# Kernel optimization log

Hardware: AMD Instinct MI355X
Metric: run time of the kernel (lower is better)

The kernel has to match this reference:

```python
import math
import jax, jax.numpy as jnp
import numpy as np

B, M, N, D, H = 64, 5, 1000, 128, 8
KS = D // H
TANH_CLIP = 10.0

def setup_inputs() -> dict:
    key = jax.random.key(0)
    ks = jax.random.split(key, 12)
    mask = jax.random.randint(ks[8], (B, M, N), 0, 2).astype(bool)
    mask = mask.at[:, 0, 0].set(True)  # guarantee at least one feasible action per batch row
    return {
        'node_embeddings': jax.random.normal(ks[0], (B, N, D), jnp.float32),
        'fixed_context': jax.random.normal(ks[1], (B, 1, D), jnp.float32),
        'prev_node_embeddings': jax.random.normal(ks[2], (B, M, D), jnp.float32),
        'node_dynamic_features': jax.random.normal(ks[3], (B, M, N, 8), jnp.float32),
        'vehicle_dynamic_features': jax.random.normal(ks[4], (B, M, 3), jnp.float32),
        'glimpse_V_static': jax.random.normal(ks[5], (H, B, 1, N, KS), jnp.float32),
        'glimpse_K_static': jax.random.normal(ks[6], (H, B, 1, N, KS), jnp.float32),
        'logit_K_static': jax.random.normal(ks[7], (B, 1, N, D), jnp.float32),
        'feasibility_mask': mask,
        'W_pcv': jax.random.normal(ks[9], (D, D + 3), jnp.float32) * 0.05,
        'W_pns': jax.random.normal(ks[10], (3 * D, 8), jnp.float32) * 0.05,
        'po_weight': jax.random.normal(ks[11], (D, D), jnp.float32) * 0.05,
    }

def reference(node_embeddings, fixed_context, prev_node_embeddings,
              node_dynamic_features, vehicle_dynamic_features,
              glimpse_V_static, glimpse_K_static, logit_K_static,
              feasibility_mask, W_pcv, W_pns, po_weight):
    # current vehicle state projection: [B,M,D]
    cvs = jnp.concatenate([prev_node_embeddings, vehicle_dynamic_features], axis=-1)
    proj_cvs = cvs @ W_pcv.T
    # dynamic node embeddings: [B,M,N,3D] -> three [B,M,N,D] chunks
    nde = node_dynamic_features @ W_pns.T
    gVd, gKd, lKd = jnp.split(nde, 3, axis=-1)
    # make heads: [B,M,N,D] -> [H,B,M,N,KS]
    def mh(x):
        return x.reshape(B, M, N, H, KS).transpose(3, 0, 1, 2, 4)
    glimpse_V = glimpse_V_static + mh(gVd)  # [H,B,M,N,KS]
    glimpse_K = glimpse_K_static + mh(gKd)
    logit_K = logit_K_static + lKd          # [B,M,N,D]
    query = fixed_context + proj_cvs        # [B,M,D]
    Q = query.reshape(B, M, H, KS).transpose(2, 0, 1, 3)  # [H,B,M,KS]
    mask_log = jnp.log(feasibility_mask.astype(jnp.float32))  # [B,M,N]
    compat = jnp.einsum('hbmk,hbmnk->hbmn', Q, glimpse_K) / math.sqrt(KS)
    compat = compat + mask_log[None]
    # softmax over joint vehicle*node axis
    attn = jax.nn.softmax(compat.reshape(H, B, M * N), axis=-1).reshape(H, B, M, N)
    heads = jnp.einsum('hbmn,hbmnk->hbmk', attn, glimpse_V)  # [H,B,M,KS]
    concat = heads.transpose(1, 2, 0, 3).reshape(B, M, D)
    final_Q = concat @ po_weight.T          # [B,M,D]
    logits = jnp.einsum('bmd,bmnd->bmn', final_Q, logit_K) / math.sqrt(D)
    logits = jnp.tanh(logits) * TANH_CLIP + mask_log
    probs = jax.nn.softmax(logits.reshape(B, M * N), axis=-1)
    return probs
```

## Files before the change

kernel.cpp:

```cpp
#include <hip/hip_runtime.h>
#include <cstddef>

#define BB 64
#define MM 5
#define NN 1000
#define DD 128
#define HH 8
#define KSZ 16
#define NCH 4
#define CH2 250
#define NC3 8
#define CH3 125
#define INV_SQRT_D 0.08838834764831845f

__device__ __forceinline__ float tanh_fast(float x) {
  float e = __expf(2.f * x);
  return 1.f - 2.f / (e + 1.f);
}

__global__ __launch_bounds__(256) void k1_query(
    const float* __restrict__ fc, const float* __restrict__ pne,
    const float* __restrict__ vdf, const float* __restrict__ wpcv,
    const float* __restrict__ wpns, const int* __restrict__ mask,
    float* __restrict__ q_ws, float* __restrict__ qw_ws,
    unsigned int* __restrict__ pmask)
{
  const int t = threadIdx.x;
  if (blockIdx.x >= BB * MM) {
    const int b = blockIdx.x - BB * MM;
    const int* mb = mask + (size_t)(b * MM) * NN;
    for (int n = t; n < NN; n += 256) {
      unsigned int pm = 0;
#pragma unroll
      for (int m = 0; m < MM; ++m) pm |= (mb[m * NN + n] != 0 ? 1u : 0u) << m;
      pmask[b * NN + n] = pm;
    }
    return;
  }
  const int bm = blockIdx.x;
  const int b = bm / MM;
  const int k = t & 15, gid = t >> 4;
  __shared__ float qsh[DD];

  float cvr[9];
  const float* pner = pne + (size_t)bm * DD;
#pragma unroll
  for (int jp = 0; jp < 8; ++jp) cvr[jp] = pner[k + 16 * jp];
  cvr[8] = (k < 3) ? vdf[bm * 3 + k] : 0.f;

#pragma unroll 2
  for (int dd = 0; dd < 8; ++dd) {
    const int d = gid + 16 * dd;
    const float* wrow = wpcv + d * 131;
    float p = 0.f;
#pragma unroll
    for (int jp = 0; jp < 8; ++jp) p = fmaf(cvr[jp], wrow[k + 16 * jp], p);
    if (k < 3) p = fmaf(cvr[8], wrow[128 + k], p);
    p += __shfl_xor(p, 1); p += __shfl_xor(p, 2);
    p += __shfl_xor(p, 4); p += __shfl_xor(p, 8);
    if (k == 0) {
      const float q = 0.25f * (p + fc[b * DD + d]);
      qsh[d] = q;
      q_ws[(size_t)bm * DD + d] = q;
    }
  }
  __syncthreads();
  if (t < 64) {
    const int h = t >> 3, f = t & 7;
    float acc = 0.f;
#pragma unroll
    for (int kk = 0; kk < KSZ; ++kk)
      acc = fmaf(qsh[h * KSZ + kk], wpns[(DD + h * KSZ + kk) * 8 + f], acc);
    qw_ws[(b * HH + h) * 40 + (bm % MM) * 8 + f] = acc;
  }
}

__global__ __launch_bounds__(256, 3) void k2_attn(
    const float* __restrict__ ndf, const float* __restrict__ gV,
    const float* __restrict__ gK, const unsigned int* __restrict__ pmask,
    const float* __restrict__ q_ws, const float* __restrict__ qw_ws,
    float* __restrict__ part)
{
  const int blk = blockIdx.x;
  const int c = blk & 3;
  const int h = (blk >> 2) & 7;
  const int b = blk >> 5;
  const int t = threadIdx.x;
  const int k = t & 3, gid = t >> 2;
  const int n0 = c * CH2;

  const float* kbase = gK + ((size_t)(h * BB + b) * NN + n0) * KSZ;
  const float* vbase = gV + ((size_t)(h * BB + b) * NN + n0) * KSZ;
  const float* nbase = ndf + ((size_t)(b * MM) * NN + n0) * 8;
  const unsigned int* pmb = pmask + b * NN + n0;

  float4 kv[4], vv[4];
  float2 ndv[4][MM];
  unsigned int pm[4];
#pragma unroll
  for (int i = 0; i < 4; ++i) {
    const int nl = gid + 64 * i;
    const bool valid = (nl < CH2);
    const int nc = valid ? nl : 0;
    pm[i] = valid ? pmb[nc] : 0u;
    kv[i] = *(const float4*)(kbase + nc * KSZ + 4 * k);
    vv[i] = *(const float4*)(vbase + nc * KSZ + 4 * k);
#pragma unroll
    for (int m = 0; m < MM; ++m)
      ndv[i][m] = *(const float2*)(nbase + ((size_t)m * NN + nc) * 8 + 2 * k);
  }

  float4 qr[MM];
  float2 qwr[MM];
#pragma unroll
  for (int m = 0; m < MM; ++m) {
    qr[m] = *(const float4*)(q_ws + (size_t)(b * MM + m) * DD + h * KSZ + 4 * k);
    qwr[m] = *(const float2*)(qw_ws + (b * HH + h) * 40 + m * 8 + 2 * k);
  }
  float4 hacc[MM] = {};
  float2 afv[MM] = {};
  float lsum = 0.f;

#pragma unroll
  for (int i = 0; i < 4; ++i) {
#pragma unroll
    for (int m = 0; m < MM; ++m) {
      float p = kv[i].x * qr[m].x + kv[i].y * qr[m].y
              + kv[i].z * qr[m].z + kv[i].w * qr[m].w
              + ndv[i][m].x * qwr[m].x + ndv[i][m].y * qwr[m].y;
      p += __shfl_xor(p, 1); p += __shfl_xor(p, 2);
      const float e = ((pm[i] >> m) & 1u) ? __expf(p) : 0.f;
      hacc[m].x = fmaf(e, vv[i].x, hacc[m].x);
      hacc[m].y = fmaf(e, vv[i].y, hacc[m].y);
      hacc[m].z = fmaf(e, vv[i].z, hacc[m].z);
      hacc[m].w = fmaf(e, vv[i].w, hacc[m].w);
      afv[m].x = fmaf(e, ndv[i][m].x, afv[m].x);
      afv[m].y = fmaf(e, ndv[i][m].y, afv[m].y);
      lsum += e;
    }
  }

#pragma unroll
  for (int m = 0; m < MM; ++m) {
#pragma unroll
    for (int off = 4; off <= 32; off <<= 1) {
      hacc[m].x += __shfl_xor(hacc[m].x, off);
      hacc[m].y += __shfl_xor(hacc[m].y, off);
      hacc[m].z += __shfl_xor(hacc[m].z, off);
      hacc[m].w += __shfl_xor(hacc[m].w, off);
      afv[m].x += __shfl_xor(afv[m].x, off);
      afv[m].y += __shfl_xor(afv[m].y, off);
    }
  }
#pragma unroll
  for (int off = 4; off <= 32; off <<= 1) lsum += __shfl_xor(lsum, off);

  __shared__ float redh[4][MM][KSZ];
  __shared__ float redaf[4][MM][8];
  __shared__ float reds[4];
  const int w = t >> 6;
  if ((t & 63) < 4) {
    const int kk = t & 3;
#pragma unroll
    for (int m = 0; m < MM; ++m) {
      redh[w][m][4 * kk + 0] = hacc[m].x;
      redh[w][m][4 * kk + 1] = hacc[m].y;
      redh[w][m][4 * kk + 2] = hacc[m].z;
      redh[w][m][4 * kk + 3] = hacc[m].w;
      redaf[w][m][2 * kk + 0] = afv[m].x;
      redaf[w][m][2 * kk + 1] = afv[m].y;
    }
  }
  if ((t & 63) == 0) reds[w] = lsum;
  __syncthreads();
  float* P = part + (size_t)blk * 128;
  if (t < 80) {
    const int m = t >> 4, kk = t & 15;
    P[t] = redh[0][m][kk] + redh[1][m][kk] + redh[2][m][kk] + redh[3][m][kk];
  } else if (t < 120) {
    const int r = t - 80, m = r >> 3, f = r & 7;
    P[80 + r] = redaf[0][m][f] + redaf[1][m][f] + redaf[2][m][f] + redaf[3][m][f];
  } else if (t == 120) {
    P[120] = reds[0] + reds[1] + reds[2] + reds[3];
  }
}

__global__ __launch_bounds__(512) void k3_logits(
    const float* __restrict__ ndf, const float* __restrict__ lK,
    const unsigned int* __restrict__ pmask, const float* __restrict__ part,
    const float* __restrict__ wpns, const float* __restrict__ po,
    float* __restrict__ out, float* __restrict__ stats)
{
  const int b = blockIdx.x >> 3;
  const int c = blockIdx.x & 7;
  const int t = threadIdx.x;

  __shared__ float pos[DD][129];
  __shared__ float rgs[HH];
  __shared__ float afs[HH][MM][8];
  __shared__ float cs[MM][DD];
  __shared__ float fqs[MM][DD];
  __shared__ float fw[MM][8];
  __shared__ float wred[8];

  for (int i = t; i < DD * DD / 4; i += 512) {
    const float4 v = ((const float4*)po)[i];
    const int r = (i * 4) >> 7, cc = (i * 4) & 127;
    pos[r][cc] = v.x; pos[r][cc + 1] = v.y; pos[r][cc + 2] = v.z; pos[r][cc + 3] = v.w;
  }
  const float* pb = part + (size_t)b * 32 * 128;
  if (t < HH) {
    float s = 0.f;
#pragma unroll
    for (int cc = 0; cc < NCH; ++cc) s += pb[(t * 4 + cc) * 128 + 120];
    rgs[t] = 1.f / s;
  }
  if (t < HH * MM * 8) {
    const int h = t / 40, r = t % 40;
    float a = 0.f;
#pragma unroll
    for (int cc = 0; cc < NCH; ++cc) a += pb[(h * 4 + cc) * 128 + 80 + r];
    afs[h][r >> 3][r & 7] = a;
  }
  __syncthreads();
  for (int idx = t; idx < MM * DD; idx += 512) {
    const int m = idx >> 7, d = idx & 127, h = d >> 4;
    float a = 0.f;
#pragma unroll
    for (int cc = 0; cc < NCH; ++cc) a += pb[(h * 4 + cc) * 128 + m * 16 + (d & 15)];
    float cf = 0.f;
#pragma unroll
    for (int f = 0; f < 8; ++f) cf = fmaf(wpns[d * 8 + f], afs[h][m][f], cf);
    cs[m][d] = (a + cf) * rgs[h];
  }
  __syncthreads();
  for (int idx = t; idx < MM * DD; idx += 512) {
    const int m = idx >> 7, d = idx & 127;
    float acc = 0.f;
#pragma unroll 8
    for (int j = 0; j < DD; ++j) acc = fmaf(cs[m][j], pos[d][j], acc);
    fqs[m][d] = acc * INV_SQRT_D;
  }
  __syncthreads();
  if (t < MM * 8) {
    const int m = t >> 3, f = t & 7;
    float acc = 0.f;
#pragma unroll 16
    for (int d = 0; d < DD; ++d) acc = fmaf(fqs[m][d], wpns[(2 * DD + d) * 8 + f], acc);
    fw[m][f] = acc;
  }
  __syncthreads();

  const int k = t & 15, gid = t >> 4;
  const int n0 = c * CH3;
  float4 fqr[MM][2];
  float fwr[MM];
#pragma unroll
  for (int m = 0; m < MM; ++m) {
    fqr[m][0] = *(const float4*)(&fqs[m][8 * k]);
    fqr[m][1] = *(const float4*)(&fqs[m][8 * k + 4]);
    fwr[m] = fw[m][k & 7];
  }
  float lsum = 0.f;

#pragma unroll
  for (int i = 0; i < 4; ++i) {
    const int nl = gid + 32 * i;
    const bool valid = (nl < CH3);
    const int n = n0 + (valid ? nl : 0);
    const unsigned int pm = valid ? pmask[b * NN + n] : 0u;
    const float* lkr = lK + ((size_t)b * NN + n) * DD;
    const float4 l0 = *(const float4*)(lkr + 8 * k);
    const float4 l1 = *(const float4*)(lkr + 8 * k + 4);
    float ndv[MM];
#pragma unroll
    for (int m = 0; m < MM; ++m)
      ndv[m] = (k < 8) ? ndf[((size_t)(b * MM + m) * NN + n) * 8 + k] : 0.f;
#pragma unroll
    for (int m = 0; m < MM; ++m) {
      float p = l0.x * fqr[m][0].x + l0.y * fqr[m][0].y
              + l0.z * fqr[m][0].z + l0.w * fqr[m][0].w
              + l1.x * fqr[m][1].x + l1.y * fqr[m][1].y
              + l1.z * fqr[m][1].z + l1.w * fqr[m][1].w
              + ndv[m] * fwr[m];
      p += __shfl_xor(p, 1); p += __shfl_xor(p, 2);
      p += __shfl_xor(p, 4); p += __shfl_xor(p, 8);
      const float e = ((pm >> m) & 1u) ? __expf(tanh_fast(p) * 10.f) : 0.f;
      if (valid) {
        lsum += e;
        if (k == 0) out[(size_t)(b * MM + m) * NN + n] = e;
      }
    }
  }
  lsum += __shfl_xor(lsum, 16);
  lsum += __shfl_xor(lsum, 32);
  if ((t & 63) == 0) wred[t >> 6] = lsum;
  __syncthreads();
  if (t == 0) {
    float s = 0.f;
#pragma unroll
    for (int w = 0; w < 8; ++w) s += wred[w];
    stats[b * NC3 + c] = s;
  }
}

__global__ __launch_bounds__(256) void k4_probs(
    const float* __restrict__ stats, float* __restrict__ out)
{
  const int bm = blockIdx.x;
  const int b = bm / MM;
  const int t = threadIdx.x;
  float s = 0.f;
#pragma unroll
  for (int c = 0; c < NC3; ++c) s += stats[b * NC3 + c];
  const float scale = 1.f / s;
  if (t < 250) {
    float4* p = (float4*)(out + (size_t)bm * NN);
    float4 v = p[t];
    v.x *= scale; v.y *= scale; v.z *= scale; v.w *= scale;
    p[t] = v;
  }
}

extern "C" void kernel_launch(void* const* d_in, const int* in_sizes, int n_in,
                              void* d_out, int out_size, void* d_ws, size_t ws_size,
                              hipStream_t stream) {
  const float* fc   = (const float*)d_in[1];
  const float* pne  = (const float*)d_in[2];
  const float* ndf  = (const float*)d_in[3];
  const float* vdf  = (const float*)d_in[4];
  const float* gV   = (const float*)d_in[5];
  const float* gK   = (const float*)d_in[6];
  const float* lK   = (const float*)d_in[7];
  const int*   mask = (const int*)d_in[8];
  const float* wpcv = (const float*)d_in[9];
  const float* wpns = (const float*)d_in[10];
  const float* po   = (const float*)d_in[11];

  float* q_ws  = (float*)d_ws;
  float* qw_ws = q_ws + BB * MM * DD;
  float* part  = qw_ws + BB * HH * MM * 8;
  float* stats = part + (size_t)BB * HH * NCH * 128;
  unsigned int* pmask = (unsigned int*)(stats + BB * NC3);
  float* out   = (float*)d_out;

  k1_query<<<BB * MM + BB, 256, 0, stream>>>(fc, pne, vdf, wpcv, wpns, mask,
                                             q_ws, qw_ws, pmask);
  k2_attn<<<BB * HH * NCH, 256, 0, stream>>>(ndf, gV, gK, pmask, q_ws, qw_ws, part);
  k3_logits<<<BB * NC3, 512, 0, stream>>>(ndf, lK, pmask, part, wpns, po, out, stats);
  k4_probs<<<BB * MM, 256, 0, stream>>>(stats, out);
}
```

Before: 56.99 us.

## Stream attention tiles through double-buffered LDS with async global-to-LDS loads

The attention kernel now assigns one block per (head, batch) pair. Each block loops over 8 node tiles, staging K, V, dynamic features and packed mask into double-buffered shared memory with global_load_lds, so loads overlap compute. This removes the 4-way node split and the partial-sum merge in the logits kernel. The query kernel is also regrouped so each block handles a quarter of D across all vehicles. The trade-off is fewer blocks (512 instead of 2048) and lower occupancy, with the tail tile clamped so it overlaps the previous data.

```diff
diff --git a/kernel.cpp b/kernel.cpp
--- a/kernel.cpp
+++ b/kernel.cpp
@@ -7,11 +7,23 @@
 #define DD 128
 #define HH 8
 #define KSZ 16
-#define NCH 4
-#define CH2 250
+#define NT 8
+#define TN 125
 #define NC3 8
 #define CH3 125
 #define INV_SQRT_D 0.08838834764831845f
+
+#define K2_KOFF 0
+#define K2_VOFF 8192
+#define K2_NOFF 16384
+#define K2_POFF 36864
+#define K2_BUF  37376
+
+typedef __attribute__((address_space(1))) const void gconst_t;
+typedef __attribute__((address_space(3))) void lds_t;
+#define GLD16(src, dst) __builtin_amdgcn_global_load_lds((gconst_t*)(src), (lds_t*)(dst), 16, 0, 0)
+#define GLD4(src, dst)  __builtin_amdgcn_global_load_lds((gconst_t*)(src), (lds_t*)(dst), 4, 0, 0)
+#define VMCNT0() asm volatile("s_waitcnt vmcnt(0)" ::: "memory")
 
 __device__ __forceinline__ float tanh_fast(float x) {
   float e = __expf(2.f * x);
@@ -26,8 +38,8 @@
     unsigned int* __restrict__ pmask)
 {
   const int t = threadIdx.x;
-  if (blockIdx.x >= BB * MM) {
-    const int b = blockIdx.x - BB * MM;
+  if (blockIdx.x >= BB * 4) {
+    const int b = blockIdx.x - BB * 4;
     const int* mb = mask + (size_t)(b * MM) * NN;
     for (int n = t; n < NN; n += 256) {
       unsigned int pm = 0;
@@ -37,20 +49,24 @@
     }
     return;
   }
-  const int bm = blockIdx.x;
-  const int b = bm / MM;
+  const int b = blockIdx.x >> 2;
+  const int dq = blockIdx.x & 3;
   const int k = t & 15, gid = t >> 4;
-  __shared__ float qsh[DD];
+  __shared__ float qsh[MM][32];
 
   float cvr[9];
-  const float* pner = pne + (size_t)bm * DD;
-#pragma unroll
-  for (int jp = 0; jp < 8; ++jp) cvr[jp] = pner[k + 16 * jp];
-  cvr[8] = (k < 3) ? vdf[bm * 3 + k] : 0.f;
-
-#pragma unroll 2
-  for (int dd = 0; dd < 8; ++dd) {
-    const int d = gid + 16 * dd;
+  int curm = -1;
+  for (int r = 0; r < 10; ++r) {
+    const int m = r >> 1;
+    if (m != curm) {
+      curm = m;
+      const float* pner = pne + (size_t)(b * MM + m) * DD;
+#pragma unroll
+      for (int jp = 0; jp < 8; ++jp) cvr[jp] = pner[k + 16 * jp];
+      cvr[8] = (k < 3) ? vdf[(b * MM + m) * 3 + k] : 0.f;
+    }
+    const int dl = (r & 1) * 16 + gid;
+    const int d = dq * 32 + dl;
     const float* wrow = wpcv + d * 131;
     float p = 0.f;
 #pragma unroll
@@ -60,120 +76,149 @@
     p += __shfl_xor(p, 4); p += __shfl_xor(p, 8);
     if (k == 0) {
       const float q = 0.25f * (p + fc[b * DD + d]);
-      qsh[d] = q;
-      q_ws[(size_t)bm * DD + d] = q;
-    }
-  }
-  __syncthreads();
-  if (t < 64) {
-    const int h = t >> 3, f = t & 7;
+      qsh[m][dl] = q;
+      q_ws[(size_t)(b * MM + m) * DD + d] = q;
+    }
+  }
+  __syncthreads();
+  if (t < 80) {
+    const int hh = t / 40;
+    const int r = t - hh * 40, m = r >> 3, f = r & 7;
+    const int h = dq * 2 + hh;
     float acc = 0.f;
 #pragma unroll
     for (int kk = 0; kk < KSZ; ++kk)
-      acc = fmaf(qsh[h * KSZ + kk], wpns[(DD + h * KSZ + kk) * 8 + f], acc);
-    qw_ws[(b * HH + h) * 40 + (bm % MM) * 8 + f] = acc;
-  }
-}
-
-__global__ __launch_bounds__(256, 3) void k2_attn(
+      acc = fmaf(qsh[m][hh * 16 + kk], wpns[(DD + h * KSZ + kk) * 8 + f], acc);
+    qw_ws[(b * HH + h) * 40 + m * 8 + f] = acc;
+  }
+}
+
+__global__ __launch_bounds__(256, 2) void k2_attn(
     const float* __restrict__ ndf, const float* __restrict__ gV,
     const float* __restrict__ gK, const unsigned int* __restrict__ pmask,
     const float* __restrict__ q_ws, const float* __restrict__ qw_ws,
     float* __restrict__ part)
 {
-  const int blk = blockIdx.x;
-  const int c = blk & 3;
-  const int h = (blk >> 2) & 7;
-  const int b = blk >> 5;
+  const int bid = blockIdx.x;
+  const int b = bid & 63;
+  const int h = bid >> 6;
   const int t = threadIdx.x;
-  const int k = t & 3, gid = t >> 2;
-  const int n0 = c * CH2;
-
-  const float* kbase = gK + ((size_t)(h * BB + b) * NN + n0) * KSZ;
-  const float* vbase = gV + ((size_t)(h * BB + b) * NN + n0) * KSZ;
-  const float* nbase = ndf + ((size_t)(b * MM) * NN + n0) * 8;
-  const unsigned int* pmb = pmask + b * NN + n0;
-
-  float4 kv[4], vv[4];
-  float2 ndv[4][MM];
-  unsigned int pm[4];
-#pragma unroll
-  for (int i = 0; i < 4; ++i) {
-    const int nl = gid + 64 * i;
-    const bool valid = (nl < CH2);
-    const int nc = valid ? nl : 0;
-    pm[i] = valid ? pmb[nc] : 0u;
-    kv[i] = *(const float4*)(kbase + nc * KSZ + 4 * k);
-    vv[i] = *(const float4*)(vbase + nc * KSZ + 4 * k);
-#pragma unroll
-    for (int m = 0; m < MM; ++m)
-      ndv[i][m] = *(const float2*)(nbase + ((size_t)m * NN + nc) * 8 + 2 * k);
-  }
-
-  float4 qr[MM];
-  float2 qwr[MM];
-#pragma unroll
-  for (int m = 0; m < MM; ++m) {
-    qr[m] = *(const float4*)(q_ws + (size_t)(b * MM + m) * DD + h * KSZ + 4 * k);
-    qwr[m] = *(const float2*)(qw_ws + (b * HH + h) * 40 + m * 8 + 2 * k);
-  }
-  float4 hacc[MM] = {};
-  float2 afv[MM] = {};
-  float lsum = 0.f;
-
-#pragma unroll
-  for (int i = 0; i < 4; ++i) {
-#pragma unroll
-    for (int m = 0; m < MM; ++m) {
-      float p = kv[i].x * qr[m].x + kv[i].y * qr[m].y
-              + kv[i].z * qr[m].z + kv[i].w * qr[m].w
-              + ndv[i][m].x * qwr[m].x + ndv[i][m].y * qwr[m].y;
-      p += __shfl_xor(p, 1); p += __shfl_xor(p, 2);
-      const float e = ((pm[i] >> m) & 1u) ? __expf(p) : 0.f;
-      hacc[m].x = fmaf(e, vv[i].x, hacc[m].x);
-      hacc[m].y = fmaf(e, vv[i].y, hacc[m].y);
-      hacc[m].z = fmaf(e, vv[i].z, hacc[m].z);
-      hacc[m].w = fmaf(e, vv[i].w, hacc[m].w);
-      afv[m].x = fmaf(e, ndv[i][m].x, afv[m].x);
-      afv[m].y = fmaf(e, ndv[i][m].y, afv[m].y);
-      lsum += e;
-    }
-  }
-
-#pragma unroll
-  for (int m = 0; m < MM; ++m) {
-#pragma unroll
-    for (int off = 4; off <= 32; off <<= 1) {
-      hacc[m].x += __shfl_xor(hacc[m].x, off);
-      hacc[m].y += __shfl_xor(hacc[m].y, off);
-      hacc[m].z += __shfl_xor(hacc[m].z, off);
-      hacc[m].w += __shfl_xor(hacc[m].w, off);
-      afv[m].x += __shfl_xor(afv[m].x, off);
-      afv[m].y += __shfl_xor(afv[m].y, off);
-    }
-  }
-#pragma unroll
-  for (int off = 4; off <= 32; off <<= 1) lsum += __shfl_xor(lsum, off);
-
+  const int w = t >> 6, lane = t & 63;
+  const int k = t & 3, g = t >> 2;
+
+  __shared__ __align__(16) char smem[2][K2_BUF];
   __shared__ float redh[4][MM][KSZ];
   __shared__ float redaf[4][MM][8];
   __shared__ float reds[4];
-  const int w = t >> 6;
-  if ((t & 63) < 4) {
-    const int kk = t & 3;
+
+  const char* gkrow = (const char*)gK + (size_t)(h * BB + b) * (NN * 64);
+  const char* gvrow = (const char*)gV + (size_t)(h * BB + b) * (NN * 64);
+  const char* pmrow = (const char*)pmask + (size_t)b * (NN * 4);
+  const char* ndrow0 = (const char*)ndf + (size_t)(b * MM) * (NN * 32);
+
+  auto stage = [&](int tt, int bb) {
+    char* base = smem[bb];
+#pragma unroll
+    for (int j = 0; j < 10; ++j) {
+      const int seg = 4 * j + w;
+      if (seg >= 38) continue;
+      if (seg < 16) {
+        const int s = seg & 7;
+        int off = tt * 8000 + s * 1024;
+        if (off > NN * 64 - 1024) off = NN * 64 - 1024;
+        const char* srow = (seg < 8) ? gkrow : gvrow;
+        const int roff = (seg < 8) ? K2_KOFF : K2_VOFF;
+        GLD16(srow + off + lane * 16, base + roff + (off - tt * 8000));
+      } else if (seg < 36) {
+        const int rel = seg - 16, m = rel >> 2, q = rel & 3;
+        int off = tt * 4000 + q * 1024;
+        if (off > NN * 32 - 1024) off = NN * 32 - 1024;
+        GLD16(ndrow0 + (size_t)m * (NN * 32) + off + lane * 16,
+              base + K2_NOFF + m * 4096 + (off - tt * 4000));
+      } else {
+        const int i4 = seg - 36;
+        int off = tt * 500 + i4 * 256;
+        if (off > NN * 4 - 256) off = NN * 4 - 256;
+        GLD4(pmrow + off + lane * 4, base + K2_POFF + (off - tt * 500));
+      }
+    }
+  };
+
+  float4 qr[MM];
+  float2 qw[MM];
+#pragma unroll
+  for (int m = 0; m < MM; ++m) {
+    qr[m] = *(const float4*)(q_ws + (size_t)(b * MM + m) * DD + h * KSZ + 4 * k);
+    qw[m] = *(const float2*)(qw_ws + (b * HH + h) * 40 + m * 8 + 2 * k);
+  }
+
+  float4 ha[MM] = {};
+  float2 af[MM] = {};
+  float ls = 0.f;
+
+  stage(0, 0);
+  VMCNT0();
+  __builtin_amdgcn_s_barrier();
+
+  for (int tt = 0; tt < NT; ++tt) {
+    const int cur = tt & 1;
+    if (tt < NT - 1) stage(tt + 1, cur ^ 1);
+    const char* base = smem[cur];
+#pragma unroll
+    for (int i = 0; i < 2; ++i) {
+      const int n = g + 64 * i;
+      if (i == 0 || g < TN - 64) {
+        const float4 kv = *(const float4*)(base + K2_KOFF + n * 64 + k * 16);
+        const float4 vv = *(const float4*)(base + K2_VOFF + n * 64 + k * 16);
+        const unsigned int pm = *(const unsigned int*)(base + K2_POFF + n * 4);
+        float2 nd[MM];
+#pragma unroll
+        for (int m = 0; m < MM; ++m)
+          nd[m] = *(const float2*)(base + K2_NOFF + m * 4096 + n * 32 + k * 8);
+#pragma unroll
+        for (int m = 0; m < MM; ++m) {
+          float p = kv.x * qr[m].x + kv.y * qr[m].y
+                  + kv.z * qr[m].z + kv.w * qr[m].w
+                  + nd[m].x * qw[m].x + nd[m].y * qw[m].y;
+          p += __shfl_xor(p, 1); p += __shfl_xor(p, 2);
+          const float e = ((pm >> m) & 1u) ? __expf(p) : 0.f;
+          ha[m].x = fmaf(e, vv.x, ha[m].x);
+          ha[m].y = fmaf(e, vv.y, ha[m].y);
+          ha[m].z = fmaf(e, vv.z, ha[m].z);
+          ha[m].w = fmaf(e, vv.w, ha[m].w);
+          af[m].x = fmaf(e, nd[m].x, af[m].x);
+          af[m].y = fmaf(e, nd[m].y, af[m].y);
+          ls += e;
+        }
+      }
+    }
+    VMCNT0();
+    __builtin_amdgcn_s_barrier();
+  }
+
+#pragma unroll
+  for (int off = 4; off <= 32; off <<= 1) {
 #pragma unroll
     for (int m = 0; m < MM; ++m) {
-      redh[w][m][4 * kk + 0] = hacc[m].x;
-      redh[w][m][4 * kk + 1] = hacc[m].y;
-      redh[w][m][4 * kk + 2] = hacc[m].z;
-      redh[w][m][4 * kk + 3] = hacc[m].w;
-      redaf[w][m][2 * kk + 0] = afv[m].x;
-      redaf[w][m][2 * kk + 1] = afv[m].y;
-    }
-  }
-  if ((t & 63) == 0) reds[w] = lsum;
-  __syncthreads();
-  float* P = part + (size_t)blk * 128;
+      ha[m].x += __shfl_xor(ha[m].x, off);
+      ha[m].y += __shfl_xor(ha[m].y, off);
+      ha[m].z += __shfl_xor(ha[m].z, off);
+      ha[m].w += __shfl_xor(ha[m].w, off);
+      af[m].x += __shfl_xor(af[m].x, off);
+      af[m].y += __shfl_xor(af[m].y, off);
+    }
+    ls += __shfl_xor(ls, off);
+  }
+  if (lane < 4) {
+#pragma unroll
+    for (int m = 0; m < MM; ++m) {
+      *(float4*)(&redh[w][m][4 * k]) = ha[m];
+      *(float2*)(&redaf[w][m][2 * k]) = af[m];
+    }
+    if (k == 0) reds[w] = ls;
+  }
+  __syncthreads();
+  float* P = part + (size_t)(b * HH + h) * 128;
   if (t < 80) {
     const int m = t >> 4, kk = t & 15;
     P[t] = redh[0][m][kk] + redh[1][m][kk] + redh[2][m][kk] + redh[3][m][kk];
@@ -208,26 +253,16 @@
     const int r = (i * 4) >> 7, cc = (i * 4) & 127;
     pos[r][cc] = v.x; pos[r][cc + 1] = v.y; pos[r][cc + 2] = v.z; pos[r][cc + 3] = v.w;
   }
-  const float* pb = part + (size_t)b * 32 * 128;
-  if (t < HH) {
-    float s = 0.f;
-#pragma unroll
-    for (int cc = 0; cc < NCH; ++cc) s += pb[(t * 4 + cc) * 128 + 120];
-    rgs[t] = 1.f / s;
-  }
+  const float* pb = part + (size_t)b * HH * 128;
+  if (t < HH) rgs[t] = 1.f / pb[t * 128 + 120];
   if (t < HH * MM * 8) {
     const int h = t / 40, r = t % 40;
-    float a = 0.f;
-#pragma unroll
-    for (int cc = 0; cc < NCH; ++cc) a += pb[(h * 4 + cc) * 128 + 80 + r];
-    afs[h][r >> 3][r & 7] = a;
+    afs[h][r >> 3][r & 7] = pb[h * 128 + 80 + r];
   }
   __syncthreads();
   for (int idx = t; idx < MM * DD; idx += 512) {
     const int m = idx >> 7, d = idx & 127, h = d >> 4;
-    float a = 0.f;
-#pragma unroll
-    for (int cc = 0; cc < NCH; ++cc) a += pb[(h * 4 + cc) * 128 + m * 16 + (d & 15)];
+    const float a = pb[h * 128 + m * 16 + (d & 15)];
     float cf = 0.f;
 #pragma unroll
     for (int f = 0; f < 8; ++f) cf = fmaf(wpns[d * 8 + f], afs[h][m][f], cf);
@@ -299,7 +334,7 @@
   if (t == 0) {
     float s = 0.f;
 #pragma unroll
-    for (int w = 0; w < 8; ++w) s += wred[w];
+    for (int w2 = 0; w2 < 8; ++w2) s += wred[w2];
     stats[b * NC3 + c] = s;
   }
 }
@@ -339,14 +374,14 @@
 
   float* q_ws  = (float*)d_ws;
   float* qw_ws = q_ws + BB * MM * DD;
-  float* part  = qw_ws + BB * HH * MM * 8;
-  float* stats = part + (size_t)BB * HH * NCH * 128;
+  float* part  = qw_ws + BB * HH * 40;
+  float* stats = part + (size_t)BB * HH * 128;
   unsigned int* pmask = (unsigned int*)(stats + BB * NC3);
   float* out   = (float*)d_out;
 
-  k1_query<<<BB * MM + BB, 256, 0, stream>>>(fc, pne, vdf, wpcv, wpns, mask,
-                                             q_ws, qw_ws, pmask);
-  k2_attn<<<BB * HH * NCH, 256, 0, stream>>>(ndf, gV, gK, pmask, q_ws, qw_ws, part);
+  k1_query<<<BB * 4 + BB, 256, 0, stream>>>(fc, pne, vdf, wpcv, wpns, mask,
+                                            q_ws, qw_ws, pmask);
+  k2_attn<<<HH * BB, 256, 0, stream>>>(ndf, gV, gK, pmask, q_ws, qw_ws, part);
   k3_logits<<<BB * NC3, 512, 0, stream>>>(ndf, lK, pmask, part, wpns, po, out, stats);
   k4_probs<<<BB * MM, 256, 0, stream>>>(stats, out);
 }
```

Result: no change. 56.78 us (-0.4%).
